# Performance work log

Hardware: AMD Instinct MI355X
Metric: run time of the kernel (lower is better)

The kernel has to match this reference:

```python
import jax, jax.numpy as jnp
import numpy as np

N = 100000      # nodes
E = 800000      # directed edges per branch
HID = 128
FOUT = 128
HEADS = 2
LAYERS = 3      # convlayer
JK_LAYERS = 3
H2 = (JK_LAYERS * HID) // 2   # PyG JK-LSTM hidden size = 192
N_AA = 26
N_SS = 3


def setup_inputs() -> dict:
    key = jax.random.key(0)
    ks = iter(jax.random.split(key, 32))
    def nrm(shape, scale=0.05):
        return jax.random.normal(next(ks), shape, dtype=jnp.float32) * scale
    return {
        "x_idx": jax.random.randint(next(ks), (N, 2), 0, N_SS),
        "x_flt": jax.random.normal(next(ks), (N, 5), dtype=jnp.float32),
        "edge_index_l": jax.random.randint(next(ks), (2, E), 0, N),
        "edge_index_r": jax.random.randint(next(ks), (2, E), 0, N),
        "emb_aa": nrm((2, N_AA, HID - 5)),          # [branch, vocab, hid-5]
        "emb_ss": nrm((2, N_SS, HID - 5)),
        "conv_W": nrm((2, LAYERS, HID, HEADS * HID)),
        "conv_att_src": nrm((2, LAYERS, HEADS, HID)),
        "conv_att_dst": nrm((2, LAYERS, HEADS, HID)),
        "conv_bias": nrm((2, LAYERS, HID)),
        "lstm_Wih": nrm((2, 2, 4 * H2, HID)),        # [branch, direction, 4H2, hid]
        "lstm_Whh": nrm((2, 2, 4 * H2, H2)),
        "lstm_bih": nrm((2, 2, 4 * H2)),
        "lstm_bhh": nrm((2, 2, 4 * H2)),
        "jk_att_W": nrm((2, 2 * H2)),
        "jk_att_b": nrm((2,)),
        "dummy_W": nrm((2, HID, HID)),
        "dummy_b": nrm((2, HID)),
        "fin_W": nrm((4, HID, FOUT)),
        "fin_b": nrm((4, FOUT)),
        "last_W": nrm((FOUT,)),                      # Linear(fout,1,bias=False)
    }


def _gat_conv(x, src, dst, W, att_src, att_dst, bias):
    # PyG GATConv, concat=False (mean over heads), leaky_relu slope 0.2
    n = x.shape[0]
    h, c = att_src.shape
    xh = (x @ W).reshape(n, h, c)                         # [N,H,C]
    a_src = jnp.einsum('nhc,hc->nh', xh, att_src)
    a_dst = jnp.einsum('nhc,hc->nh', xh, att_dst)
    e = jax.nn.leaky_relu(a_src[src] + a_dst[dst], 0.2)   # [E,H]
    m = jax.ops.segment_max(e, dst, num_segments=n)
    ex = jnp.exp(e - m[dst])
    denom = jax.ops.segment_sum(ex, dst, num_segments=n)
    alpha = ex / (denom[dst] + 1e-16)                     # segment softmax over dst
    out = jax.ops.segment_sum(xh[src] * alpha[:, :, None], dst, num_segments=n)
    return out.mean(axis=1) + bias                        # [N,C]


def _lstm_dir(xs, Wih, Whh, bih, bhh, reverse):
    # xs: [L,N,C]; single-layer LSTM, torch gate order i,f,g,o
    n = xs.shape[1]
    h2 = Whh.shape[1]
    b = bih + bhh
    def cell(carry, xt):
        h, c = carry
        g = xt @ Wih.T + h @ Whh.T + b
        i, f, gg, o = jnp.split(g, 4, axis=-1)
        c = jax.nn.sigmoid(f) * c + jax.nn.sigmoid(i) * jnp.tanh(gg)
        h = jax.nn.sigmoid(o) * jnp.tanh(c)
        return (h, c), h
    init = (jnp.zeros((n, h2), xs.dtype), jnp.zeros((n, h2), xs.dtype))
    _, hs = jax.lax.scan(cell, init, xs, reverse=reverse)
    return hs  # [L,N,H2]


def _jk(xs, Wih, Whh, bih, bhh, att_w, att_b):
    # PyG JumpingKnowledge('lstm'): bi-LSTM over layer axis + scalar attention
    hf = _lstm_dir(xs, Wih[0], Whh[0], bih[0], bhh[0], False)
    hb = _lstm_dir(xs, Wih[1], Whh[1], bih[1], bhh[1], True)
    h = jnp.concatenate([hf, hb], axis=-1)                # [L,N,2H2]
    a = jax.nn.softmax(jnp.einsum('lnh,h->ln', h, att_w) + att_b, axis=0)
    return (xs * a[..., None]).sum(axis=0)                # [N,C]


def _forward(x_idx, x_flt, edge_index_l, edge_index_r, emb_aa, emb_ss,
             conv_W, conv_att_src, conv_att_dst, conv_bias,
             lstm_Wih, lstm_Whh, lstm_bih, lstm_bhh, jk_att_W, jk_att_b,
             dummy_W, dummy_b, fin_W, fin_b, last_W):
    n = x_idx.shape[0]
    loops = jnp.arange(n)  # GATConv add_self_loops=True
    src_l = jnp.concatenate([edge_index_l[0], loops]); dst_l = jnp.concatenate([edge_index_l[1], loops])
    src_r = jnp.concatenate([edge_index_r[0], loops]); dst_r = jnp.concatenate([edge_index_r[1], loops])
    x_l = jnp.concatenate([emb_aa[0][x_idx[:, 0]] + emb_ss[0][x_idx[:, 1]], x_flt], axis=1)
    x_r = jnp.concatenate([emb_aa[1][x_idx[:, 0]] + emb_ss[1][x_idx[:, 1]], x_flt], axis=1)
    xs_l, xs_r = [], []
    for i in range(LAYERS):
        mean = (x_l + x_r) * 0.5
        o_l = mean + jax.nn.relu(_gat_conv(x_l, src_l, dst_l, conv_W[0, i], conv_att_src[0, i], conv_att_dst[0, i], conv_bias[0, i]))
        o_r = mean + jax.nn.relu(_gat_conv(x_r, src_r, dst_r, conv_W[1, i], conv_att_src[1, i], conv_att_dst[1, i], conv_bias[1, i]))
        x_l, x_r = o_l, o_r
        xs_l.append(x_l); xs_r.append(x_r)
    jk_l = _jk(jnp.stack(xs_l), lstm_Wih[0], lstm_Whh[0], lstm_bih[0], lstm_bhh[0], jk_att_W[0], jk_att_b[0])
    jk_r = _jk(jnp.stack(xs_r), lstm_Wih[1], lstm_Whh[1], lstm_bih[1], lstm_bhh[1], jk_att_W[1], jk_att_b[1])
    sq_l = jk_l @ dummy_W[0] + dummy_b[0]
    sq_r = jk_r @ dummy_W[1] + dummy_b[1]
    feats = [jk_l, sq_l, jk_r, sq_r]
    outs = [feats[i] @ fin_W[i] + fin_b[i] for i in range(4)]
    alpha = jax.nn.softmax(jnp.stack([o @ last_W for o in outs], axis=1), axis=1)  # [N,4]
    nodeemb = sum(outs[i] * alpha[:, i:i + 1] for i in range(4))
    return nodeemb


def reference(x_idx, x_flt, edge_index_l, edge_index_r, emb_aa, emb_ss,
              conv_W, conv_att_src, conv_att_dst, conv_bias,
              lstm_Wih, lstm_Whh, lstm_bih, lstm_bhh, jk_att_W, jk_att_b,
              dummy_W, dummy_b, fin_W, fin_b, last_W):
    return _forward(x_idx, x_flt, edge_index_l, edge_index_r, emb_aa, emb_ss,
                    conv_W, conv_att_src, conv_att_dst, conv_bias,
                    lstm_Wih, lstm_Whh, lstm_bih, lstm_bhh, jk_att_W, jk_att_b,
                    dummy_W, dummy_b, fin_W, fin_b, last_W)
```

## Files before the change

### kernel.cpp

```cpp
#include <hip/hip_runtime.h>
#include <cstddef>
#include <cstdint>

#define N_NODES 100000
#define N_EDGES 800000
#define EL_TOT  900000
#define HID 128
#define H2  192
#define G4  768
#define CH3 50000
#define BK  32
#define LDST 32
#define SCANB 98

typedef unsigned short bf16;
typedef __attribute__((ext_vector_type(8))) short bf16x8v;
typedef __attribute__((ext_vector_type(4))) float f32x4v;

#define AS1 __attribute__((address_space(1)))
#define AS3 __attribute__((address_space(3)))

__device__ __forceinline__ void async16(const bf16* g, bf16* l) {
    __builtin_amdgcn_global_load_lds((AS1 void*)g, (AS3 void*)l, 16, 0, 0);
}
// ... 109 lines not shown
        __syncthreads();
    }
    if (i < N_NODES) tmp[i] = sdata[threadIdx.x];
    if (threadIdx.x == 1023) bsums[b * SCANB + blockIdx.x] = sdata[1023];
}

__global__ void scan2_kernel(int* __restrict__ bsums) {
    int b = threadIdx.x;
    if (b < 2) {
        int c = 0;
        for (int k = 0; k < SCANB; ++k) {
            int t = bsums[b * SCANB + k];
            bsums[b * SCANB + k] = c;
            c += t;
        }
    }
}

__global__ void scan3_kernel(const int* __restrict__ bsums,
                             const int* __restrict__ deg0, const int* __restrict__ deg1,
                             const int* __restrict__ tmp0, const int* __restrict__ tmp1,
                             int* __restrict__ offs0, int* __restrict__ offs1,
                             int* __restrict__ pos0, int* __restrict__ pos1) {
    const int b = blockIdx.y;
    const int* deg = b ? deg1 : deg0;
    const int* tmp = b ? tmp1 : tmp0;
    int* offs = b ? offs1 : offs0;
    int* pos = b ? pos1 : pos0;
    int carry = bsums[b * SCANB + blockIdx.x];
    int i = blockIdx.x * 1024 + threadIdx.x;
    if (i < N_NODES) {
        int inc = tmp[i] + carry;
        offs[i + 1] = inc;
        pos[i] = inc - deg[i];
    }
    if (i == 0) offs[0] = 0;
}

__global__ void fill_kernel(const int* __restrict__ srcrow,
                            const int* __restrict__ dstrow,
                            int* __restrict__ pos, int* __restrict__ srcs) {
    int t = blockIdx.x * blockDim.x + threadIdx.x;
    if (t >= EL_TOT) return;
    int s, d;
    if (t < N_EDGES) { s = srcrow[t]; d = dstrow[t]; }
    else             { s = d = t - N_EDGES; }
    int p = atomicAdd(&pos[d], 1);
    srcs[p] = s;
}

template<typename TC>
__device__ __forceinline__ void gemm128_body(
    const bf16* __restrict__ A1, const bf16* __restrict__ B1, int K1,
    const bf16* __restrict__ A2, const bf16* __restrict__ B2, int K2,
    TC* __restrict__ C, const float* __restrict__ bias, int R, int M,
    int bm0, int bn0) {
    __shared__ bf16 As[2][128 * LDST];
    __shared__ bf16 Bs[2][128 * LDST];
    const int tid = threadIdx.x;
    const int lane = tid & 63;
    const int wave = tid >> 6;
    const int wm = (wave & 1) * 64, wn = (wave >> 1) * 64;
    const int l15 = lane & 15;
    const int q8 = (lane >> 4) * 8;
    const int lr = lane >> 2;
    const int lc = (lane & 3) * 8;

    f32x4v acc[4][4];
#pragma unroll
    for (int i = 0; i < 4; ++i)
#pragma unroll
        for (int j = 0; j < 4; ++j) acc[i][j] = (f32x4v)(0.0f);

    const int n1 = K1 / BK;
    const int n2 = A2 ? (K2 / BK) : 0;
    const int ns = n1 + n2;

    auto stage = [&](int buf, int s) {
        const bf16* Ap; const bf16* Bp; int K, k0;
        if (s < n1) { Ap = A1; Bp = B1; K = K1; k0 = s * BK; }
        else        { Ap = A2; Bp = B2; K = K2; k0 = (s - n1) * BK; }
#pragma unroll
        for (int rnd = 0; rnd < 2; ++rnd) {
            const int rbase = wave * 16 + rnd * 64;
            const int row = rbase + lr;
            int ga = bm0 + row; ga = (ga < R) ? ga : (R - 1);
            async16(Ap + (size_t)ga * K + k0 + lc, &As[buf][rbase * LDST]);
            async16(Bp + (size_t)(bn0 + row) * K + k0 + lc, &Bs[buf][rbase * LDST]);
        }
    };

    stage(0, 0);
    __syncthreads();
    for (int s = 0; s < ns; ++s) {
        const int cur = s & 1;
        if (s + 1 < ns) stage(cur ^ 1, s + 1);
        bf16x8v af[4], bfv[4];
#pragma unroll
        for (int i = 0; i < 4; ++i) {
            af[i]  = *(const bf16x8v*)&As[cur][(wm + i * 16 + l15) * LDST + q8];
            bfv[i] = *(const bf16x8v*)&Bs[cur][(wn + i * 16 + l15) * LDST + q8];
        }
#pragma unroll
        for (int i = 0; i < 4; ++i)
#pragma unroll
            for (int j = 0; j < 4; ++j)
                acc[i][j] = __builtin_amdgcn_mfma_f32_16x16x32_bf16(
                    af[i], bfv[j], acc[i][j], 0, 0, 0);
        __syncthreads();
    }

#pragma unroll
    for (int i = 0; i < 4; ++i) {
        const int row0 = bm0 + wm + i * 16 + (lane >> 4) * 4;
#pragma unroll
        for (int j = 0; j < 4; ++j) {
            const int col = bn0 + wn + j * 16 + l15;
            const float bv = bias ? bias[col] : 0.f;
#pragma unroll
            for (int r = 0; r < 4; ++r) {
                const int gr = row0 + r;
                if (gr < R) stE(C, (size_t)gr * M + col, acc[i][j][r] + bv);
            }
        }
    }
}

template<typename TC>
__global__ __launch_bounds__(256) void mfma_gemm_kernel(
    const bf16* __restrict__ A1, const bf16* __restrict__ B1, int K1,
    const bf16* __restrict__ A2, const bf16* __restrict__ B2, int K2,
    TC* __restrict__ C, const float* __restrict__ bias, int R, int M) {
    int bm0, nt;
    if (!swz_tile(R, M >> 7, bm0, nt)) return;
    gemm128_body<TC>(A1, B1, K1, A2, B2, K2, C, bias, R, M, bm0, nt * 128);
}

template<typename TC>
__global__ __launch_bounds__(256) void mfma_gemm_b_kernel(
    const bf16* a0, const bf16* a1, const bf16* a2, const bf16* a3,
    const bf16* __restrict__ Bbase,
    TC* c0, TC* c1, TC* c2, TC* c3,
    const float* __restrict__ bias, int R) {
    int bm0, nt;
    if (!swz_tile(R, 1, bm0, nt)) return;
    const int y = blockIdx.y;
    const bf16* A1 = (y == 0) ? a0 : (y == 1) ? a1 : (y == 2) ? a2 : a3;
    TC* C = (y == 0) ? c0 : (y == 1) ? c1 : (y == 2) ? c2 : c3;
    gemm128_body<TC>(A1, Bbase + (size_t)y * 128 * 128, 128,
                     nullptr, nullptr, 0, C,
                     bias + (size_t)y * 128, R, 128, bm0, 0);
}

__global__ __launch_bounds__(256) void lstm_gemm_kernel(
    const bf16* __restrict__ A1, const bf16* __restrict__ B1,
    const bf16* __restrict__ A2, const bf16* __restrict__ B2,
    const float* __restrict__ bias, bf16* __restrict__ c_state,
    bf16* __restrict__ h_out, const float* __restrict__ aw,
    float* __restrict__ score, int R) {
    __shared__ bf16 As[2][128 * LDST];
    __shared__ bf16 Bs[2][128 * LDST];
    int bm0, nt;
    if (!swz_tile(R, G4 >> 7, bm0, nt)) return;
    const int bn0 = nt * 128;
    const int tid = threadIdx.x;
    const int lane = tid & 63;
    const int wave = tid >> 6;
    const int wm = (wave & 1) * 64, wn = (wave >> 1) * 64;
    const int l15 = lane & 15;
    const int q = lane >> 4;
    const int q8 = q * 8;
    const int lr = lane >> 2;
    const int lc = (lane & 3) * 8;
    const bool first = (A2 == nullptr);

    f32x4v acc[4][4];
#pragma unroll
    for (int i = 0; i < 4; ++i)
#pragma unroll
        for (int j = 0; j < 4; ++j) acc[i][j] = (f32x4v)(0.0f);

    const int n1 = HID / BK;
    const int ns = n1 + (first ? 0 : (H2 / BK));

    auto stage = [&](int buf, int s) {
        const bf16* Ap; const bf16* Bp; int K, k0;
        if (s < n1) { Ap = A1; Bp = B1; K = HID; k0 = s * BK; }
        else        { Ap = A2; Bp = B2; K = H2;  k0 = (s - n1) * BK; }
#pragma unroll
        for (int rnd = 0; rnd < 2; ++rnd) {
            const int rbase = wave * 16 + rnd * 64;
            const int row = rbase + lr;
            int ga = bm0 + row; ga = (ga < R) ? ga : (R - 1);
            async16(Ap + (size_t)ga * K + k0 + lc, &As[buf][rbase * LDST]);
            async16(Bp + (size_t)(bn0 + row) * K + k0 + lc, &Bs[buf][rbase * LDST]);
        }
    };

    stage(0, 0);
    __syncthreads();
    for (int s = 0; s < ns; ++s) {
        const int cur = s & 1;
        if (s + 1 < ns) stage(cur ^ 1, s + 1);
        bf16x8v af[4], bfv[4];
#pragma unroll
        for (int i = 0; i < 4; ++i) {
            af[i]  = *(const bf16x8v*)&As[cur][(wm + i * 16 + l15) * LDST + q8];
            bfv[i] = *(const bf16x8v*)&Bs[cur][(wn + i * 16 + l15) * LDST + q8];
        }
#pragma unroll
        for (int i = 0; i < 4; ++i)
#pragma unroll
            for (int j = 0; j < 4; ++j)
                acc[i][j] = __builtin_amdgcn_mfma_f32_16x16x32_bf16(
                    af[i], bfv[j], acc[i][j], 0, 0, 0);
        __syncthreads();
    }

    const int u = ((bn0 + wn) >> 6) * 16 + l15;
    const float awu = aw[u];
    float bv[4];
#pragma unroll
    for (int j = 0; j < 4; ++j) bv[j] = bias[bn0 + wn + j * 16 + l15];
    float psum[4][4];
#pragma unroll
    for (int i = 0; i < 4; ++i) {
        const int row0 = bm0 + wm + i * 16 + q * 4;
#pragma unroll
        for (int r = 0; r < 4; ++r) {
            const int gr = row0 + r;
            const bool ok = gr < R;
            float ig = acc[i][0][r] + bv[0];
            float fg = acc[i][1][r] + bv[1];
            float gg = acc[i][2][r] + bv[2];
            float og = acc[i][3][r] + bv[3];
            float si = 1.f / (1.f + __expf(-ig));
            float sf = 1.f / (1.f + __expf(-fg));
            float so = 1.f / (1.f + __expf(-og));
            float co = (ok && !first) ? b2f(c_state[(size_t)gr * H2 + u]) : 0.f;
            float cn = sf * co + si * ftanh(gg);
            float hn = so * ftanh(cn);
            if (ok) {
                c_state[(size_t)gr * H2 + u] = f2b(cn);
                h_out[(size_t)gr * H2 + u] = f2b(hn);
            }
            psum[i][r] = hn * awu;
        }
    }
#pragma unroll
    for (int m = 1; m < 16; m <<= 1)
#pragma unroll
        for (int i = 0; i < 4; ++i)
#pragma unroll
            for (int r = 0; r < 4; ++r)
                psum[i][r] += __shfl_xor(psum[i][r], m);
    if (l15 == 0) {
#pragma unroll
        for (int i = 0; i < 4; ++i)
#pragma unroll
            for (int r = 0; r < 4; ++r) {
                const int gr = bm0 + wm + i * 16 + q * 4 + r;
                if (gr < R) atomicAdd(&score[gr], psum[i][r]);
            }
    }
}

__global__ __launch_bounds__(256) void mfma_gemm_x0_kernel(
    const int* __restrict__ xidx, const float* __restrict__ xflt,
    const float* __restrict__ embA, const float* __restrict__ embS,
    const bf16* __restrict__ B1, bf16* __restrict__ C, int R, int M) {
    __shared__ bf16 As[128 * LDST];
    __shared__ bf16 Bs[128 * LDST];
    int bm0, nt;
    if (!swz_tile(R, M >> 7, bm0, nt)) return;
    const int bn0 = nt * 128;
    const int tid = threadIdx.x;
    const int lane = tid & 63;
    const int wave = tid >> 6;
    const int wm = (wave & 1) * 64, wn = (wave >> 1) * 64;
    const int l15 = lane & 15;
    const int q8 = (lane >> 4) * 8;
    const int srow = tid >> 2;
    const int scol = (tid & 3) * 8;
    const int lr = lane >> 2;
    const int lc = (lane & 3) * 8;

    f32x4v acc[4][4];
#pragma unroll
    for (int i = 0; i < 4; ++i)
#pragma unroll
        for (int j = 0; j < 4; ++j) acc[i][j] = (f32x4v)(0.0f);

    for (int k0 = 0; k0 < 128; k0 += BK) {
#pragma unroll
        for (int rnd = 0; rnd < 2; ++rnd) {
            {
                int row = srow + rnd * 64;
                int ga = bm0 + row; ga = (ga < R) ? ga : (R - 1);
                int ia = xidx[2 * ga], is_ = xidx[2 * ga + 1];
                bf16 tmp[8];
#pragma unroll
                for (int t = 0; t < 8; ++t)
                    tmp[t] = f2b(x0_val(k0 + scol + t, ia, is_, ga, embA, embS, xflt));
                *(int4*)&As[row * LDST + scol] = *(const int4*)tmp;
            }
            {
                const int rbase = wave * 16 + rnd * 64;
                int row = rbase + lr;
                async16(B1 + (size_t)(bn0 + row) * 128 + k0 + lc, &Bs[rbase * LDST]);
            }
        }
        __syncthreads();
        bf16x8v af[4], bfv[4];
#pragma unroll
        for (int i = 0; i < 4; ++i) {
            af[i]  = *(const bf16x8v*)&As[(wm + i * 16 + l15) * LDST + q8];
            bfv[i] = *(const bf16x8v*)&Bs[(wn + i * 16 + l15) * LDST + q8];
        }
#pragma unroll
        for (int i = 0; i < 4; ++i)
#pragma unroll
            for (int j = 0; j < 4; ++j)
                acc[i][j] = __builtin_amdgcn_mfma_f32_16x16x32_bf16(
                    af[i], bfv[j], acc[i][j], 0, 0, 0);
        __syncthreads();
    }
#pragma unroll
    for (int i = 0; i < 4; ++i) {
        const int row0 = bm0 + wm + i * 16 + (lane >> 4) * 4;
#pragma unroll
        for (int j = 0; j < 4; ++j) {
            const int col = bn0 + wn + j * 16 + l15;
#pragma unroll
            for (int r = 0; r < 4; ++r) {
                const int gr = row0 + r;
                if (gr < R) C[(size_t)gr * M + col] = f2b(acc[i][j][r]);
            }
        }
    }
}


__global__ __launch_bounds__(256) void att_kernel(
    const bf16* __restrict__ xh, const float* __restrict__ as_,
    const float* __restrict__ ad_, float* __restrict__ asrc, float* __restrict__ adst) {
    int w = (blockIdx.x * blockDim.x + threadIdx.x) >> 6;
    int lane = threadIdx.x & 63;
    if (w >= N_NODES) return;
    const bf16* row = xh + (size_t)w * 256;
    float x0 = b2f(row[lane]), x1 = b2f(row[64 + lane]);
    float x2 = b2f(row[128 + lane]), x3 = b2f(row[192 + lane]);
    float s0 = x0 * as_[lane] + x1 * as_[64 + lane];
    float s1 = x2 * as_[128 + lane] + x3 * as_[192 + lane];
    float d0 = x0 * ad_[lane] + x1 * ad_[64 + lane];
    float d1 = x2 * ad_[128 + lane] + x3 * ad_[192 + lane];
    for (int o = 1; o < 64; o <<= 1) {
        s0 += __shfl_xor(s0, o); s1 += __shfl_xor(s1, o);
        d0 += __shfl_xor(d0, o); d1 += __shfl_xor(d1, o);
    }
    if (lane == 0) {
        asrc[2 * w] = s0; asrc[2 * w + 1] = s1;
        adst[2 * w] = d0; adst[2 * w + 1] = d1;
    }
}

__device__ __forceinline__ float lrelu02(float x) { return x > 0.f ? x : 0.2f * x; }

__global__ __launch_bounds__(256) void agg_kernel(
    const bf16* __restrict__ xh, const float* __restrict__ asrc,
    const float* __restrict__ adst, const int* __restrict__ offs,
    const int* __restrict__ srcs,
    const bf16* __restrict__ xprev_l, const bf16* __restrict__ xprev_r,
    const int* __restrict__ xidx, const float* __restrict__ xflt,
    const float* __restrict__ embAl, const float* __restrict__ embSl,
    const float* __restrict__ embAr, const float* __restrict__ embSr,
    const float* __restrict__ bias, bf16* __restrict__ outx) {
    int n = (blockIdx.x * blockDim.x + threadIdx.x) >> 6;
    int lane = threadIdx.x & 63;
    if (n >= N_NODES) return;
    const int start = offs[n], end = offs[n + 1];
    const float ad0 = adst[2 * n], ad1 = adst[2 * n + 1];

    const int eh = lane >> 5;
    const int l32 = lane & 31;
    const int head = l32 >> 4;
    const int l15 = l32 & 15;
    const int col = head * 128 + l15 * 8;
    const float adh = head ? ad1 : ad0;

    float acc[8] = {0.f, 0.f, 0.f, 0.f, 0.f, 0.f, 0.f, 0.f};
    float dsum = 0.f;
#pragma unroll 2
    for (int j = start; j < end; j += 2) {
        int e = j + eh;
        if (e < end) {
            int s = srcs[e];
            float a = asrc[2 * s + head] + adh;
            float al = __expf(lrelu02(a));
            if (l15 == 0) dsum += al;
            int4 v = *(const int4*)(xh + (size_t)s * 256 + col);
            const int* w = (const int*)&v;
#pragma unroll
            for (int t = 0; t < 4; ++t) {
                float lo = __uint_as_float(((unsigned)w[t]) << 16);
                float hi = __uint_as_float(((unsigned)w[t]) & 0xffff0000u);
                acc[2 * t]     += lo * al;
                acc[2 * t + 1] += hi * al;
            }
        }
    }
#pragma unroll
    for (int t = 0; t < 8; ++t) acc[t] += __shfl_xor(acc[t], 32);
    dsum += __shfl_xor(dsum, 32);
    float dh = __shfl(dsum, lane & 48);
    float invh = 1.f / (dh + 1e-16f);
#pragma unroll
    for (int t = 0; t < 8; ++t) {
        acc[t] *= invh;
        acc[t] = 0.5f * (acc[t] + __shfl_xor(acc[t], 16));
    }

    if (lane < 16) {
        const int c0 = lane * 8;
        const size_t base = (size_t)n * HID + c0;
        float xm[8];
        if (xidx) {
            int ia = xidx[2 * n], is_ = xidx[2 * n + 1];
#pragma unroll
            for (int t = 0; t < 8; ++t)
                xm[t] = 0.5f * (x0_val(c0 + t, ia, is_, n, embAl, embSl, xflt) +
                                x0_val(c0 + t, ia, is_, n, embAr, embSr, xflt));
        } else {
            int4 vl = *(const int4*)(xprev_l + base);
            int4 vr = *(const int4*)(xprev_r + base);
            const int* wl = (const int*)&vl;
            const int* wr = (const int*)&vr;
#pragma unroll
            for (int t = 0; t < 4; ++t) {
                xm[2 * t] = 0.5f * (__uint_as_float(((unsigned)wl[t]) << 16) +
                                    __uint_as_float(((unsigned)wr[t]) << 16));
                xm[2 * t + 1] = 0.5f * (__uint_as_float(((unsigned)wl[t]) & 0xffff0000u) +
                                        __uint_as_float(((unsigned)wr[t]) & 0xffff0000u));
            }
        }
        bf16 res[8];
#pragma unroll
        for (int t = 0; t < 8; ++t)
            res[t] = f2b(xm[t] + fmaxf(0.f, acc[t] + bias[c0 + t]));
        *(int4*)(outx + base) = *(const int4*)res;
    }
}


__global__ __launch_bounds__(256) void jkfin_kernel(
    const float* __restrict__ sb, const bf16* __restrict__ xs0,
    const bf16* __restrict__ xs1, const bf16* __restrict__ xs2,
    bf16* __restrict__ jk) {
    int w = (blockIdx.x * blockDim.x + threadIdx.x) >> 6;
    int lane = threadIdx.x & 63;
    if (w >= N_NODES) return;
    float s0 = sb[w], s1 = sb[N_NODES + w], s2 = sb[2 * N_NODES + w];
    float m = fmaxf(s0, fmaxf(s1, s2));
    float a0 = __expf(s0 - m), a1 = __expf(s1 - m), a2 = __expf(s2 - m);
    float inv = 1.f / (a0 + a1 + a2);
    a0 *= inv; a1 *= inv; a2 *= inv;
    size_t gn = (size_t)w * HID + lane * 2;
#pragma unroll
    for (int t = 0; t < 2; ++t) {
        float v0 = b2f(xs0[gn + t]);
        float v1 = b2f(xs1[gn + t]);
        float v2 = b2f(xs2[gn + t]);
        jk[gn + t] = f2b(v0 * a0 + v1 * a1 + v2 * a2);
    }
}

__global__ __launch_bounds__(256) void final_kernel(
    const float* __restrict__ o0, const float* __restrict__ o1,
    const float* __restrict__ o2, const float* __restrict__ o3,
    const float* __restrict__ lw, float* __restrict__ out, int nloc, long long c3off) {
    int w = (blockIdx.x * blockDim.x + threadIdx.x) >> 6;
    int lane = threadIdx.x & 63;
    if (w >= nloc) return;
    size_t base = (size_t)w * HID;
    float w0 = lw[lane], w1 = lw[64 + lane];
    const float* op[4] = {o0, o1, o2, o3};
    float v[4][2];
    float s[4];
#pragma unroll
    for (int i = 0; i < 4; ++i) {
        v[i][0] = op[i][base + lane];
        v[i][1] = op[i][base + 64 + lane];
        float t = v[i][0] * w0 + v[i][1] * w1;
        for (int o = 1; o < 64; o <<= 1) t += __shfl_xor(t, o);
        s[i] = t;
    }
    float m = fmaxf(fmaxf(s[0], s[1]), fmaxf(s[2], s[3]));
    float e0 = __expf(s[0] - m), e1 = __expf(s[1] - m);
    float e2 = __expf(s[2] - m), e3 = __expf(s[3] - m);
    float inv = 1.f / (e0 + e1 + e2 + e3);
    float r0 = (v[0][0] * e0 + v[1][0] * e1 + v[2][0] * e2 + v[3][0] * e3) * inv;
    float r1 = (v[0][1] * e0 + v[1][1] * e1 + v[2][1] * e2 + v[3][1] * e3) * inv;
    size_t obase = (size_t)(c3off + w) * HID;
    out[obase + lane] = r0;
    out[obase + 64 + lane] = r1;
}


static long long align1k(long long x) { return (x + 1023) & ~1023LL; }

extern "C" void kernel_launch(void* const* d_in, const int* in_sizes, int n_in,
                              void* d_out, int out_size, void* d_ws, size_t ws_size,
                              hipStream_t stream) {
    (void)in_sizes; (void)n_in; (void)out_size;
    const int*   x_idx   = (const int*)  d_in[0];
    const float* x_flt   = (const float*)d_in[1];
    const int*   ei_l    = (const int*)  d_in[2];
    const int*   ei_r    = (const int*)  d_in[3];
    const float* emb_aa  = (const float*)d_in[4];
    const float* emb_ss  = (const float*)d_in[5];
    const float* conv_W  = (const float*)d_in[6];
    const float* att_s   = (const float*)d_in[7];
    const float* att_d   = (const float*)d_in[8];
    const float* conv_b  = (const float*)d_in[9];
    const float* Wih     = (const float*)d_in[10];
    const float* Whh     = (const float*)d_in[11];
    const float* bih     = (const float*)d_in[12];
    const float* bhh     = (const float*)d_in[13];
    const float* jkw     = (const float*)d_in[14];
    const float* dummy_W = (const float*)d_in[16];
    const float* dummy_b = (const float*)d_in[17];
    const float* fin_W   = (const float*)d_in[18];
    const float* fin_b   = (const float*)d_in[19];
    const float* last_W  = (const float*)d_in[20];
    float* out = (float*)d_out;

    const long long S = (long long)N_NODES * HID;
    char* ws = (char*)d_ws;
    long long off = 0;

    bf16* hist = (bf16*)(ws + off);  off += align1k(6 * S * 2);
    float* scores = (float*)(ws + off); off += align1k(6LL * N_NODES * 4);
    float* bsum   = (float*)(ws + off); off += align1k(4LL * G4 * 4);
    int* bsums    = (int*)(ws + off);  off += align1k(2LL * SCANB * 4);
    bf16* Wih_b   = (bf16*)(ws + off); off += align1k(4LL * G4 * HID * 2);
    bf16* Whh_b   = (bf16*)(ws + off); off += align1k(4LL * G4 * H2 * 2);
    bf16* dummyWt = (bf16*)(ws + off); off += align1k(2LL * 128 * 128 * 2);
    bf16* finWt   = (bf16*)(ws + off); off += align1k(4LL * 128 * 128 * 2);

    char* BIG = ws + off;
    const long long slot0 = align1k(2 * S * 2);
    const long long slot1 = align1k((long long)N_NODES * H2 * 2);
    const long long need = off + slot0 + slot1;

    if ((long long)ws_size < need) {
        float val = 200000.0f + (float)(ws_size >> 20);
        sentinel_kernel<<<(N_NODES * HID + 255) / 256, 256, 0, stream>>>(
            out, N_NODES * HID, val);
        return;
    }

    bf16* xh  = (bf16*)BIG;
    bf16* jkb = (bf16*)BIG;
    int* ibase = (int*)(BIG + slot0);
    int *deg[2], *offs[2], *pos[2], *srcs[2];
    long long io = 0;
    for (int b = 0; b < 2; ++b) {
        deg[b]  = ibase + io; io += N_NODES;
        offs[b] = ibase + io; io += N_NODES + 1;
        pos[b]  = ibase + io; io += N_NODES;
        srcs[b] = ibase + io; io += EL_TOT;
    }
    long long io4a = ((io * 4 + 15) & ~15LL);
    float* asrc = (float*)(BIG + slot0 + io4a);
    float* adst = asrc + 2LL * N_NODES;
    bf16* convWt = (bf16*)(BIG + slot0 + io4a + 4LL * N_NODES * 4);
    bf16* hA = (bf16*)BIG;
    bf16* hB = (bf16*)d_out;
    bf16* cC = (bf16*)(BIG + slot0);

    const float* embA[2] = {emb_aa, emb_aa + 26 * 123};
    const float* embS[2] = {emb_ss, emb_ss + 3 * 123};

    bsum_perm_kernel<<<12, 256, 0, stream>>>(bih, bhh, bsum);
    trans_kernel<<<(6 * 128 * 256 + 255) / 256, 256, 0, stream>>>(
        conv_W, convWt, 6, 128, 256);
    lstm_w_perm_kernel<<<(4 * G4 * HID + 255) / 256, 256, 0, stream>>>(
        Wih, Wih_b, HID);
    lstm_w_perm_kernel<<<(4 * G4 * H2 + 255) / 256, 256, 0, stream>>>(
        Whh, Whh_b, H2);
    trans_kernel<<<(2 * 128 * 128 + 255) / 256, 256, 0, stream>>>(
        dummy_W, dummyWt, 2, 128, 128);
    trans_kernel<<<(4 * 128 * 128 + 255) / 256, 256, 0, stream>>>(
        fin_W, finWt, 4, 128, 128);
    hipMemsetAsync(deg[0], 0, N_NODES * sizeof(int), stream);
    hipMemsetAsync(deg[1], 0, N_NODES * sizeof(int), stream);
    deg_kernel<<<(EL_TOT + 255) / 256, 256, 0, stream>>>(ei_l + N_EDGES, deg[0]);
    deg_kernel<<<(EL_TOT + 255) / 256, 256, 0, stream>>>(ei_r + N_EDGES, deg[1]);
    scan1_kernel<<<dim3(SCANB, 2), 1024, 0, stream>>>(
        deg[0], deg[1], pos[0], pos[1], bsums);
    scan2_kernel<<<1, 64, 0, stream>>>(bsums);
    scan3_kernel<<<dim3(SCANB, 2), 1024, 0, stream>>>(
        bsums, deg[0], deg[1], pos[0], pos[1], offs[0], offs[1], pos[0], pos[1]);
    fill_kernel<<<(EL_TOT + 255) / 256, 256, 0, stream>>>(
        ei_l, ei_l + N_EDGES, pos[0], srcs[0]);
    fill_kernel<<<(EL_TOT + 255) / 256, 256, 0, stream>>>(
        ei_r, ei_r + N_EDGES, pos[1], srcs[1]);

    for (int i = 0; i < 3; ++i) {
        for (int b = 0; b < 2; ++b) {
            const bf16* Wc = convWt + (size_t)(b * 3 + i) * 256 * 128;
            if (i == 0) {
                mfma_gemm_x0_kernel<<<swz_grid(N_NODES, 2), 256, 0, stream>>>(
                    x_idx, x_flt, embA[b], embS[b], Wc, xh, N_NODES, 256);
            } else {
                mfma_gemm_kernel<bf16><<<swz_grid(N_NODES, 2), 256, 0, stream>>>(
                    hist + (size_t)(b * 3 + i - 1) * S, Wc, 128,
                    nullptr, nullptr, 0, xh, nullptr, N_NODES, 256);
            }
            att_kernel<<<25000, 256, 0, stream>>>(
                xh, att_s + (size_t)(b * 3 + i) * 2 * HID,
                att_d + (size_t)(b * 3 + i) * 2 * HID, asrc, adst);
            const bf16* xpl = (i == 0) ? nullptr : hist + (size_t)(i - 1) * S;
            const bf16* xpr = (i == 0) ? nullptr : hist + (size_t)(3 + i - 1) * S;
            agg_kernel<<<25000, 256, 0, stream>>>(
                xh, asrc, adst, offs[b], srcs[b], xpl, xpr,
                (i == 0) ? x_idx : nullptr, x_flt,
                embA[0], embS[0], embA[1], embS[1],
                conv_b + (size_t)(b * 3 + i) * HID, hist + (size_t)(b * 3 + i) * S);
        }
    }

    hipMemsetAsync(scores, 0, (size_t)6 * N_NODES * 4, stream);
    const int gx = swz_grid(N_NODES, 6);
    for (int b = 0; b < 2; ++b) {
        for (int dir = 0; dir < 2; ++dir) {
            const bf16* Wi = Wih_b + (size_t)(b * 2 + dir) * G4 * HID;
            const bf16* Wh = Whh_b + (size_t)(b * 2 + dir) * G4 * H2;
            const float* bs = bsum + (size_t)(b * 2 + dir) * G4;
            const float* aw = jkw + (size_t)b * 2 * H2 + (size_t)dir * H2;
            for (int st = 0; st < 3; ++st) {
                int l = dir ? (2 - st) : st;
                const bf16* A = hist + (size_t)(b * 3 + l) * S;
                const bf16* hin = (st == 0) ? nullptr : ((st & 1) ? hA : hB);
                bf16* hout = (st & 1) ? hB : hA;
                lstm_gemm_kernel<<<gx, 256, 0, stream>>>(
                    A, Wi, hin, Wh, bs, cC, hout, aw,
                    scores + (size_t)(b * 3 + l) * N_NODES, N_NODES);
            }
        }
    }
    for (int b = 0; b < 2; ++b)
        jkfin_kernel<<<25000, 256, 0, stream>>>(
            scores + (size_t)b * 3 * N_NODES,
            hist + (size_t)b * 3 * S, hist + (size_t)(b * 3 + 1) * S,
            hist + (size_t)(b * 3 + 2) * S, jkb + (size_t)b * S);

    float* f3 = (float*)hist;
    bf16* jkl = jkb; bf16* jkr = jkb + S;
    for (long long c3 = 0; c3 < N_NODES; c3 += CH3) {
        int Rr = (int)((N_NODES - c3) < CH3 ? (N_NODES - c3) : CH3);
        float* o0 = f3;
        float* o1 = f3 + 1LL * CH3 * HID;
        float* o2 = f3 + 2LL * CH3 * HID;
        float* o3 = f3 + 3LL * CH3 * HID;
        bf16* sql = (bf16*)(f3 + 4LL * CH3 * HID);
        bf16* sqr = sql + (long long)CH3 * HID;
        mfma_gemm_b_kernel<bf16><<<dim3(swz_grid(Rr, 1), 2), 256, 0, stream>>>(
            jkl + c3 * HID, jkr + c3 * HID, nullptr, nullptr,
            dummyWt, sql, sqr, nullptr, nullptr, dummy_b, Rr);
        mfma_gemm_b_kernel<float><<<dim3(swz_grid(Rr, 1), 4), 256, 0, stream>>>(
            jkl + c3 * HID, sql, jkr + c3 * HID, sqr,
            finWt, o0, o1, o2, o3, fin_b, Rr);
        final_kernel<<<(Rr + 3) / 4, 256, 0, stream>>>(
            o0, o1, o2, o3, last_W, out, Rr, c3);
    }
}
```

Baseline: 3.014 ms.

## Fuse attention logits into aggregation and batch LSTM directions per launch

Removes the separate att_kernel. The aggregation kernel now recomputes the per-edge source attention logit from the gathered source row and the destination logit from the node's own row, and each wave processes four edges at a time across both heads. The LSTM GEMM launches are also merged so the forward and backward directions of a branch run in one 2-D grid, when the workspace is large enough to hold separate state buffers per direction. The cost is redundant dot products and shuffles on every edge, plus higher register pressure in the aggregation kernel.

```diff
diff --git a/kernel.cpp b/kernel.cpp
--- a/kernel.cpp
+++ b/kernel.cpp
@@ -285,17 +285,32 @@
                      bias + (size_t)y * 128, R, 128, bm0, 0);
 }
 
-__global__ __launch_bounds__(256) void lstm_gemm_kernel(
-    const bf16* __restrict__ A1, const bf16* __restrict__ B1,
-    const bf16* __restrict__ A2, const bf16* __restrict__ B2,
-    const float* __restrict__ bias, bf16* __restrict__ c_state,
-    bf16* __restrict__ h_out, const float* __restrict__ aw,
-    float* __restrict__ score, int R) {
+__global__ __launch_bounds__(256) void lstm_gemm2_kernel(
+    const bf16* __restrict__ Ax0, const bf16* __restrict__ Ax1,
+    const bf16* __restrict__ Wi, const bf16* __restrict__ Wh,
+    const float* __restrict__ biasB,
+    bf16* __restrict__ cS0, bf16* __restrict__ cS1,
+    const bf16* __restrict__ hin0, const bf16* __restrict__ hin1,
+    bf16* __restrict__ hout0, bf16* __restrict__ hout1,
+    const float* __restrict__ awB,
+    float* __restrict__ score0, float* __restrict__ score1,
+    int first, int R) {
     __shared__ bf16 As[2][128 * LDST];
     __shared__ bf16 Bs[2][128 * LDST];
     int bm0, nt;
     if (!swz_tile(R, G4 >> 7, bm0, nt)) return;
     const int bn0 = nt * 128;
+    const int y = blockIdx.y;
+    const bf16* A1 = y ? Ax1 : Ax0;
+    const bf16* B1 = Wi + (size_t)y * G4 * HID;
+    const bf16* A2 = y ? hin1 : hin0;
+    const bf16* B2 = Wh + (size_t)y * G4 * H2;
+    const float* bias = biasB + (size_t)y * G4;
+    bf16* c_state = y ? cS1 : cS0;
+    bf16* h_out = y ? hout1 : hout0;
+    const float* aw = awB + (size_t)y * H2;
+    float* score = y ? score1 : score0;
+
     const int tid = threadIdx.x;
     const int lane = tid & 63;
     const int wave = tid >> 6;
@@ -305,7 +320,6 @@
     const int q8 = q * 8;
     const int lr = lane >> 2;
     const int lc = (lane & 3) * 8;
-    const bool first = (A2 == nullptr);
 
     f32x4v acc[4][4];
 #pragma unroll
@@ -474,34 +488,11 @@
 }
 
 
-__global__ __launch_bounds__(256) void att_kernel(
+__device__ __forceinline__ float lrelu02(float x) { return x > 0.f ? x : 0.2f * x; }
+
+__global__ __launch_bounds__(256) void agg_kernel(
     const bf16* __restrict__ xh, const float* __restrict__ as_,
-    const float* __restrict__ ad_, float* __restrict__ asrc, float* __restrict__ adst) {
-    int w = (blockIdx.x * blockDim.x + threadIdx.x) >> 6;
-    int lane = threadIdx.x & 63;
-    if (w >= N_NODES) return;
-    const bf16* row = xh + (size_t)w * 256;
-    float x0 = b2f(row[lane]), x1 = b2f(row[64 + lane]);
-    float x2 = b2f(row[128 + lane]), x3 = b2f(row[192 + lane]);
-    float s0 = x0 * as_[lane] + x1 * as_[64 + lane];
-    float s1 = x2 * as_[128 + lane] + x3 * as_[192 + lane];
-    float d0 = x0 * ad_[lane] + x1 * ad_[64 + lane];
-    float d1 = x2 * ad_[128 + lane] + x3 * ad_[192 + lane];
-    for (int o = 1; o < 64; o <<= 1) {
-        s0 += __shfl_xor(s0, o); s1 += __shfl_xor(s1, o);
-        d0 += __shfl_xor(d0, o); d1 += __shfl_xor(d1, o);
-    }
-    if (lane == 0) {
-        asrc[2 * w] = s0; asrc[2 * w + 1] = s1;
-        adst[2 * w] = d0; adst[2 * w + 1] = d1;
-    }
-}
-
-__device__ __forceinline__ float lrelu02(float x) { return x > 0.f ? x : 0.2f * x; }
-
-__global__ __launch_bounds__(256) void agg_kernel(
-    const bf16* __restrict__ xh, const float* __restrict__ asrc,
-    const float* __restrict__ adst, const int* __restrict__ offs,
+    const float* __restrict__ ad_, const int* __restrict__ offs,
     const int* __restrict__ srcs,
     const bf16* __restrict__ xprev_l, const bf16* __restrict__ xprev_r,
     const int* __restrict__ xidx, const float* __restrict__ xflt,
@@ -512,49 +503,84 @@
     int lane = threadIdx.x & 63;
     if (n >= N_NODES) return;
     const int start = offs[n], end = offs[n + 1];
-    const float ad0 = adst[2 * n], ad1 = adst[2 * n + 1];
-
-    const int eh = lane >> 5;
-    const int l32 = lane & 31;
-    const int head = l32 >> 4;
-    const int l15 = l32 & 15;
-    const int col = head * 128 + l15 * 8;
-    const float adh = head ? ad1 : ad0;
-
-    float acc[8] = {0.f, 0.f, 0.f, 0.f, 0.f, 0.f, 0.f, 0.f};
-    float dsum = 0.f;
+    const int l15 = lane & 15;
+    const int g = lane >> 4;
+
+    float av0[8], av1[8];
+#pragma unroll
+    for (int t = 0; t < 8; ++t) {
+        av0[t] = as_[l15 * 8 + t];
+        av1[t] = as_[128 + l15 * 8 + t];
+    }
+
+    float d0, d1;
+    {
+        uint2 v = *(const uint2*)(xh + (size_t)n * 256 + lane * 4);
+        float p = ad_[lane * 4 + 0] * b2f((bf16)(v.x & 0xffffu))
+                + ad_[lane * 4 + 1] * b2f((bf16)(v.x >> 16))
+                + ad_[lane * 4 + 2] * b2f((bf16)(v.y & 0xffffu))
+                + ad_[lane * 4 + 3] * b2f((bf16)(v.y >> 16));
+        for (int o = 1; o < 32; o <<= 1) p += __shfl_xor(p, o);
+        d0 = __shfl(p, 0);
+        d1 = __shfl(p, 32);
+    }
+
+    float acc0[8] = {0, 0, 0, 0, 0, 0, 0, 0};
+    float acc1[8] = {0, 0, 0, 0, 0, 0, 0, 0};
+    float ds0 = 0.f, ds1 = 0.f;
 #pragma unroll 2
-    for (int j = start; j < end; j += 2) {
-        int e = j + eh;
+    for (int j = start; j < end; j += 4) {
+        int e = j + g;
         if (e < end) {
             int s = srcs[e];
-            float a = asrc[2 * s + head] + adh;
-            float al = __expf(lrelu02(a));
-            if (l15 == 0) dsum += al;
-            int4 v = *(const int4*)(xh + (size_t)s * 256 + col);
-            const int* w = (const int*)&v;
+            const bf16* row = xh + (size_t)s * 256 + l15 * 8;
+            int4 v0 = *(const int4*)row;
+            int4 v1 = *(const int4*)(row + 128);
+            const int* w0 = (const int*)&v0;
+            const int* w1 = (const int*)&v1;
+            float x0[8], x1[8];
 #pragma unroll
             for (int t = 0; t < 4; ++t) {
-                float lo = __uint_as_float(((unsigned)w[t]) << 16);
-                float hi = __uint_as_float(((unsigned)w[t]) & 0xffff0000u);
-                acc[2 * t]     += lo * al;
-                acc[2 * t + 1] += hi * al;
-            }
-        }
-    }
-#pragma unroll
-    for (int t = 0; t < 8; ++t) acc[t] += __shfl_xor(acc[t], 32);
-    dsum += __shfl_xor(dsum, 32);
-    float dh = __shfl(dsum, lane & 48);
-    float invh = 1.f / (dh + 1e-16f);
+                x0[2 * t]     = __uint_as_float(((unsigned)w0[t]) << 16);
+                x0[2 * t + 1] = __uint_as_float(((unsigned)w0[t]) & 0xffff0000u);
+                x1[2 * t]     = __uint_as_float(((unsigned)w1[t]) << 16);
+                x1[2 * t + 1] = __uint_as_float(((unsigned)w1[t]) & 0xffff0000u);
+            }
+            float p0 = 0.f, p1 = 0.f;
+#pragma unroll
+            for (int t = 0; t < 8; ++t) { p0 += av0[t] * x0[t]; p1 += av1[t] * x1[t]; }
+#pragma unroll
+            for (int m = 1; m < 16; m <<= 1) {
+                p0 += __shfl_xor(p0, m);
+                p1 += __shfl_xor(p1, m);
+            }
+            float al0 = __expf(lrelu02(p0 + d0));
+            float al1 = __expf(lrelu02(p1 + d1));
+            if (l15 == 0) { ds0 += al0; ds1 += al1; }
+#pragma unroll
+            for (int t = 0; t < 8; ++t) {
+                acc0[t] += x0[t] * al0;
+                acc1[t] += x1[t] * al1;
+            }
+        }
+    }
 #pragma unroll
     for (int t = 0; t < 8; ++t) {
-        acc[t] *= invh;
-        acc[t] = 0.5f * (acc[t] + __shfl_xor(acc[t], 16));
-    }
+        acc0[t] += __shfl_xor(acc0[t], 16); acc0[t] += __shfl_xor(acc0[t], 32);
+        acc1[t] += __shfl_xor(acc1[t], 16); acc1[t] += __shfl_xor(acc1[t], 32);
+    }
+    ds0 += __shfl_xor(ds0, 16); ds0 += __shfl_xor(ds0, 32);
+    ds1 += __shfl_xor(ds1, 16); ds1 += __shfl_xor(ds1, 32);
+    ds0 = __shfl(ds0, 0); ds1 = __shfl(ds1, 0);
+    const float inv0 = 1.f / (ds0 + 1e-16f);
+    const float inv1 = 1.f / (ds1 + 1e-16f);
+    float accm[8];
+#pragma unroll
+    for (int t = 0; t < 8; ++t)
+        accm[t] = 0.5f * (acc0[t] * inv0 + acc1[t] * inv1);
 
     if (lane < 16) {
-        const int c0 = lane * 8;
+        const int c0 = l15 * 8;
         const size_t base = (size_t)n * HID + c0;
         float xm[8];
         if (xidx) {
@@ -579,7 +605,7 @@
         bf16 res[8];
 #pragma unroll
         for (int t = 0; t < 8; ++t)
-            res[t] = f2b(xm[t] + fmaxf(0.f, acc[t] + bias[c0 + t]));
+            res[t] = f2b(xm[t] + fmaxf(0.f, accm[t] + bias[c0 + t]));
         *(int4*)(outx + base) = *(const int4*)res;
     }
 }
@@ -683,14 +709,17 @@
     char* BIG = ws + off;
     const long long slot0 = align1k(2 * S * 2);
     const long long slot1 = align1k((long long)N_NODES * H2 * 2);
-    const long long need = off + slot0 + slot1;
-
-    if ((long long)ws_size < need) {
+    const long long HS    = slot1;
+    const long long need_seq = off + slot0 + slot1;
+    const long long need_tB  = off + 5 * HS;
+
+    if ((long long)ws_size < need_seq) {
         float val = 200000.0f + (float)(ws_size >> 20);
         sentinel_kernel<<<(N_NODES * HID + 255) / 256, 256, 0, stream>>>(
             out, N_NODES * HID, val);
         return;
     }
+    const bool tierB = (long long)ws_size >= need_tB;
 
     bf16* xh  = (bf16*)BIG;
     bf16* jkb = (bf16*)BIG;
@@ -704,12 +733,16 @@
         srcs[b] = ibase + io; io += EL_TOT;
     }
     long long io4a = ((io * 4 + 15) & ~15LL);
-    float* asrc = (float*)(BIG + slot0 + io4a);
-    float* adst = asrc + 2LL * N_NODES;
-    bf16* convWt = (bf16*)(BIG + slot0 + io4a + 4LL * N_NODES * 4);
+    bf16* convWt = (bf16*)(BIG + slot0 + io4a);
     bf16* hA = (bf16*)BIG;
     bf16* hB = (bf16*)d_out;
     bf16* cC = (bf16*)(BIG + slot0);
+    bf16* cB0 = (bf16*)BIG;
+    bf16* cB1 = (bf16*)(BIG + HS);
+    bf16* hX0 = (bf16*)(BIG + 2 * HS);
+    bf16* hX1 = (bf16*)(BIG + 3 * HS);
+    bf16* hY0 = (bf16*)(BIG + 4 * HS);
+    bf16* hY1 = (bf16*)d_out;
 
     const float* embA[2] = {emb_aa, emb_aa + 26 * 123};
     const float* embS[2] = {emb_ss, emb_ss + 3 * 123};
@@ -750,13 +783,12 @@
                     hist + (size_t)(b * 3 + i - 1) * S, Wc, 128,
                     nullptr, nullptr, 0, xh, nullptr, N_NODES, 256);
             }
-            att_kernel<<<25000, 256, 0, stream>>>(
-                xh, att_s + (size_t)(b * 3 + i) * 2 * HID,
-                att_d + (size_t)(b * 3 + i) * 2 * HID, asrc, adst);
             const bf16* xpl = (i == 0) ? nullptr : hist + (size_t)(i - 1) * S;
             const bf16* xpr = (i == 0) ? nullptr : hist + (size_t)(3 + i - 1) * S;
             agg_kernel<<<25000, 256, 0, stream>>>(
-                xh, asrc, adst, offs[b], srcs[b], xpl, xpr,
+                xh, att_s + (size_t)(b * 3 + i) * 2 * HID,
+                att_d + (size_t)(b * 3 + i) * 2 * HID,
+                offs[b], srcs[b], xpl, xpr,
                 (i == 0) ? x_idx : nullptr, x_flt,
                 embA[0], embS[0], embA[1], embS[1],
                 conv_b + (size_t)(b * 3 + i) * HID, hist + (size_t)(b * 3 + i) * S);
@@ -765,20 +797,44 @@
 
     hipMemsetAsync(scores, 0, (size_t)6 * N_NODES * 4, stream);
     const int gx = swz_grid(N_NODES, 6);
-    for (int b = 0; b < 2; ++b) {
-        for (int dir = 0; dir < 2; ++dir) {
-            const bf16* Wi = Wih_b + (size_t)(b * 2 + dir) * G4 * HID;
-            const bf16* Wh = Whh_b + (size_t)(b * 2 + dir) * G4 * H2;
-            const float* bs = bsum + (size_t)(b * 2 + dir) * G4;
-            const float* aw = jkw + (size_t)b * 2 * H2 + (size_t)dir * H2;
+    if (tierB) {
+        for (int b = 0; b < 2; ++b) {
+            const int c0 = b * 2;
             for (int st = 0; st < 3; ++st) {
-                int l = dir ? (2 - st) : st;
-                const bf16* A = hist + (size_t)(b * 3 + l) * S;
-                const bf16* hin = (st == 0) ? nullptr : ((st & 1) ? hA : hB);
-                bf16* hout = (st & 1) ? hB : hA;
-                lstm_gemm_kernel<<<gx, 256, 0, stream>>>(
-                    A, Wi, hin, Wh, bs, cC, hout, aw,
-                    scores + (size_t)(b * 3 + l) * N_NODES, N_NODES);
+                const int l0 = st, l1 = 2 - st;
+                const bf16 *hin0, *hin1; bf16 *ho0, *ho1;
+                if (st == 0)      { hin0 = hin1 = nullptr; ho0 = hX0; ho1 = hX1; }
+                else if (st == 1) { hin0 = hX0; hin1 = hX1; ho0 = hY0; ho1 = hY1; }
+                else              { hin0 = hY0; hin1 = hY1; ho0 = hX0; ho1 = hX1; }
+                lstm_gemm2_kernel<<<dim3(gx, 2), 256, 0, stream>>>(
+                    hist + (size_t)(b * 3 + l0) * S, hist + (size_t)(b * 3 + l1) * S,
+                    Wih_b + (size_t)c0 * G4 * HID, Whh_b + (size_t)c0 * G4 * H2,
+                    bsum + (size_t)c0 * G4,
+                    cB0, cB1, hin0, hin1, ho0, ho1,
+                    jkw + (size_t)b * 2 * H2,
+                    scores + (size_t)(b * 3 + l0) * N_NODES,
+                    scores + (size_t)(b * 3 + l1) * N_NODES,
+                    st == 0 ? 1 : 0, N_NODES);
+            }
+        }
+    } else {
+        for (int b = 0; b < 2; ++b) {
+            for (int dir = 0; dir < 2; ++dir) {
+                const int combo = b * 2 + dir;
+                for (int st = 0; st < 3; ++st) {
+                    int l = dir ? (2 - st) : st;
+                    const bf16* hin = (st == 0) ? nullptr : ((st & 1) ? hA : hB);
+                    bf16* hout = (st & 1) ? hB : hA;
+                    lstm_gemm2_kernel<<<dim3(gx, 1), 256, 0, stream>>>(
+                        hist + (size_t)(b * 3 + l) * S, nullptr,
+                        Wih_b + (size_t)combo * G4 * HID,
+                        Whh_b + (size_t)combo * G4 * H2,
+                        bsum + (size_t)combo * G4,
+                        cC, nullptr, hin, nullptr, hout, nullptr,
+                        jkw + (size_t)b * 2 * H2 + (size_t)dir * H2,
+                        scores + (size_t)(b * 3 + l) * N_NODES, nullptr,
+                        st == 0 ? 1 : 0, N_NODES);
+                }
             }
         }
     }
```

After: 2.998 ms. No clear change (-0.5%).

## Fuse dst-attention into aggregation, process both heads per edge, skip last LSTM stores

Applied to the files above, without the earlier changes.

Removes the destination-attention dot product and its buffer from att_kernel and recomputes it inside agg_kernel from the node's own xh row. The aggregation loop is restructured so each lane group handles one edge for both heads (4 edges in flight per wave instead of 2 edges split by head), loading asrc as a float2. The LSTM kernel gets explicit first/last flags and skips writing c_state and h_out on the final step, which nothing reads. The unused second-operand path in gemm128_body is also removed.

```diff
diff --git a/kernel.cpp b/kernel.cpp
--- a/kernel.cpp
+++ b/kernel.cpp
@@ -185,7 +185,6 @@
 template<typename TC>
 __device__ __forceinline__ void gemm128_body(
     const bf16* __restrict__ A1, const bf16* __restrict__ B1, int K1,
-    const bf16* __restrict__ A2, const bf16* __restrict__ B2, int K2,
     TC* __restrict__ C, const float* __restrict__ bias, int R, int M,
     int bm0, int bn0) {
     __shared__ bf16 As[2][128 * LDST];
@@ -205,21 +204,16 @@
 #pragma unroll
         for (int j = 0; j < 4; ++j) acc[i][j] = (f32x4v)(0.0f);
 
-    const int n1 = K1 / BK;
-    const int n2 = A2 ? (K2 / BK) : 0;
-    const int ns = n1 + n2;
-
+    const int ns = K1 / BK;
     auto stage = [&](int buf, int s) {
-        const bf16* Ap; const bf16* Bp; int K, k0;
-        if (s < n1) { Ap = A1; Bp = B1; K = K1; k0 = s * BK; }
-        else        { Ap = A2; Bp = B2; K = K2; k0 = (s - n1) * BK; }
+        const int k0 = s * BK;
 #pragma unroll
         for (int rnd = 0; rnd < 2; ++rnd) {
             const int rbase = wave * 16 + rnd * 64;
             const int row = rbase + lr;
             int ga = bm0 + row; ga = (ga < R) ? ga : (R - 1);
-            async16(Ap + (size_t)ga * K + k0 + lc, &As[buf][rbase * LDST]);
-            async16(Bp + (size_t)(bn0 + row) * K + k0 + lc, &Bs[buf][rbase * LDST]);
+            async16(A1 + (size_t)ga * K1 + k0 + lc, &As[buf][rbase * LDST]);
+            async16(B1 + (size_t)(bn0 + row) * K1 + k0 + lc, &Bs[buf][rbase * LDST]);
         }
     };
 
@@ -262,11 +256,10 @@
 template<typename TC>
 __global__ __launch_bounds__(256) void mfma_gemm_kernel(
     const bf16* __restrict__ A1, const bf16* __restrict__ B1, int K1,
-    const bf16* __restrict__ A2, const bf16* __restrict__ B2, int K2,
     TC* __restrict__ C, const float* __restrict__ bias, int R, int M) {
     int bm0, nt;
     if (!swz_tile(R, M >> 7, bm0, nt)) return;
-    gemm128_body<TC>(A1, B1, K1, A2, B2, K2, C, bias, R, M, bm0, nt * 128);
+    gemm128_body<TC>(A1, B1, K1, C, bias, R, M, bm0, nt * 128);
 }
 
 template<typename TC>
@@ -280,8 +273,7 @@
     const int y = blockIdx.y;
     const bf16* A1 = (y == 0) ? a0 : (y == 1) ? a1 : (y == 2) ? a2 : a3;
     TC* C = (y == 0) ? c0 : (y == 1) ? c1 : (y == 2) ? c2 : c3;
-    gemm128_body<TC>(A1, Bbase + (size_t)y * 128 * 128, 128,
-                     nullptr, nullptr, 0, C,
+    gemm128_body<TC>(A1, Bbase + (size_t)y * 128 * 128, 128, C,
                      bias + (size_t)y * 128, R, 128, bm0, 0);
 }
 
@@ -290,7 +282,7 @@
     const bf16* __restrict__ A2, const bf16* __restrict__ B2,
     const float* __restrict__ bias, bf16* __restrict__ c_state,
     bf16* __restrict__ h_out, const float* __restrict__ aw,
-    float* __restrict__ score, int R) {
+    float* __restrict__ score, int first, int last, int R) {
     __shared__ bf16 As[2][128 * LDST];
     __shared__ bf16 Bs[2][128 * LDST];
     int bm0, nt;
@@ -305,7 +297,6 @@
     const int q8 = q * 8;
     const int lr = lane >> 2;
     const int lc = (lane & 3) * 8;
-    const bool first = (A2 == nullptr);
 
     f32x4v acc[4][4];
 #pragma unroll
@@ -373,7 +364,7 @@
             float co = (ok && !first) ? b2f(c_state[(size_t)gr * H2 + u]) : 0.f;
             float cn = sf * co + si * ftanh(gg);
             float hn = so * ftanh(cn);
-            if (ok) {
+            if (ok && !last) {
                 c_state[(size_t)gr * H2 + u] = f2b(cn);
                 h_out[(size_t)gr * H2 + u] = f2b(hn);
             }
@@ -476,7 +467,7 @@
 
 __global__ __launch_bounds__(256) void att_kernel(
     const bf16* __restrict__ xh, const float* __restrict__ as_,
-    const float* __restrict__ ad_, float* __restrict__ asrc, float* __restrict__ adst) {
+    float* __restrict__ asrc) {
     int w = (blockIdx.x * blockDim.x + threadIdx.x) >> 6;
     int lane = threadIdx.x & 63;
     if (w >= N_NODES) return;
@@ -485,15 +476,11 @@
     float x2 = b2f(row[128 + lane]), x3 = b2f(row[192 + lane]);
     float s0 = x0 * as_[lane] + x1 * as_[64 + lane];
     float s1 = x2 * as_[128 + lane] + x3 * as_[192 + lane];
-    float d0 = x0 * ad_[lane] + x1 * ad_[64 + lane];
-    float d1 = x2 * ad_[128 + lane] + x3 * ad_[192 + lane];
     for (int o = 1; o < 64; o <<= 1) {
         s0 += __shfl_xor(s0, o); s1 += __shfl_xor(s1, o);
-        d0 += __shfl_xor(d0, o); d1 += __shfl_xor(d1, o);
     }
     if (lane == 0) {
         asrc[2 * w] = s0; asrc[2 * w + 1] = s1;
-        adst[2 * w] = d0; adst[2 * w + 1] = d1;
     }
 }
 
@@ -501,7 +488,7 @@
 
 __global__ __launch_bounds__(256) void agg_kernel(
     const bf16* __restrict__ xh, const float* __restrict__ asrc,
-    const float* __restrict__ adst, const int* __restrict__ offs,
+    const float* __restrict__ ad_, const int* __restrict__ offs,
     const int* __restrict__ srcs,
     const bf16* __restrict__ xprev_l, const bf16* __restrict__ xprev_r,
     const int* __restrict__ xidx, const float* __restrict__ xflt,
@@ -512,49 +499,64 @@
     int lane = threadIdx.x & 63;
     if (n >= N_NODES) return;
     const int start = offs[n], end = offs[n + 1];
-    const float ad0 = adst[2 * n], ad1 = adst[2 * n + 1];
-
-    const int eh = lane >> 5;
-    const int l32 = lane & 31;
-    const int head = l32 >> 4;
-    const int l15 = l32 & 15;
-    const int col = head * 128 + l15 * 8;
-    const float adh = head ? ad1 : ad0;
-
-    float acc[8] = {0.f, 0.f, 0.f, 0.f, 0.f, 0.f, 0.f, 0.f};
-    float dsum = 0.f;
+    const int l15 = lane & 15;
+    const int g = lane >> 4;
+
+    float d0, d1;
+    {
+        uint2 v = *(const uint2*)(xh + (size_t)n * 256 + lane * 4);
+        float p = ad_[lane * 4 + 0] * b2f((bf16)(v.x & 0xffffu))
+                + ad_[lane * 4 + 1] * b2f((bf16)(v.x >> 16))
+                + ad_[lane * 4 + 2] * b2f((bf16)(v.y & 0xffffu))
+                + ad_[lane * 4 + 3] * b2f((bf16)(v.y >> 16));
+        for (int o = 1; o < 32; o <<= 1) p += __shfl_xor(p, o);
+        d0 = __shfl(p, 0);
+        d1 = __shfl(p, 32);
+    }
+
+    float acc0[8] = {0, 0, 0, 0, 0, 0, 0, 0};
+    float acc1[8] = {0, 0, 0, 0, 0, 0, 0, 0};
+    float ds0 = 0.f, ds1 = 0.f;
 #pragma unroll 2
-    for (int j = start; j < end; j += 2) {
-        int e = j + eh;
+    for (int j = start; j < end; j += 4) {
+        int e = j + g;
         if (e < end) {
             int s = srcs[e];
-            float a = asrc[2 * s + head] + adh;
-            float al = __expf(lrelu02(a));
-            if (l15 == 0) dsum += al;
-            int4 v = *(const int4*)(xh + (size_t)s * 256 + col);
-            const int* w = (const int*)&v;
+            float2 a2 = *(const float2*)(asrc + 2 * s);
+            float al0 = __expf(lrelu02(a2.x + d0));
+            float al1 = __expf(lrelu02(a2.y + d1));
+            if (l15 == 0) { ds0 += al0; ds1 += al1; }
+            const bf16* row = xh + (size_t)s * 256 + l15 * 8;
+            int4 v0 = *(const int4*)row;
+            int4 v1 = *(const int4*)(row + 128);
+            const int* w0 = (const int*)&v0;
+            const int* w1 = (const int*)&v1;
 #pragma unroll
             for (int t = 0; t < 4; ++t) {
-                float lo = __uint_as_float(((unsigned)w[t]) << 16);
-                float hi = __uint_as_float(((unsigned)w[t]) & 0xffff0000u);
-                acc[2 * t]     += lo * al;
-                acc[2 * t + 1] += hi * al;
-            }
-        }
-    }
-#pragma unroll
-    for (int t = 0; t < 8; ++t) acc[t] += __shfl_xor(acc[t], 32);
-    dsum += __shfl_xor(dsum, 32);
-    float dh = __shfl(dsum, lane & 48);
-    float invh = 1.f / (dh + 1e-16f);
+                acc0[2 * t]     += __uint_as_float(((unsigned)w0[t]) << 16) * al0;
+                acc0[2 * t + 1] += __uint_as_float(((unsigned)w0[t]) & 0xffff0000u) * al0;
+                acc1[2 * t]     += __uint_as_float(((unsigned)w1[t]) << 16) * al1;
+                acc1[2 * t + 1] += __uint_as_float(((unsigned)w1[t]) & 0xffff0000u) * al1;
+            }
+        }
+    }
 #pragma unroll
     for (int t = 0; t < 8; ++t) {
-        acc[t] *= invh;
-        acc[t] = 0.5f * (acc[t] + __shfl_xor(acc[t], 16));
-    }
+        acc0[t] += __shfl_xor(acc0[t], 16); acc0[t] += __shfl_xor(acc0[t], 32);
+        acc1[t] += __shfl_xor(acc1[t], 16); acc1[t] += __shfl_xor(acc1[t], 32);
+    }
+    ds0 += __shfl_xor(ds0, 16); ds0 += __shfl_xor(ds0, 32);
+    ds1 += __shfl_xor(ds1, 16); ds1 += __shfl_xor(ds1, 32);
+    ds0 = __shfl(ds0, 0); ds1 = __shfl(ds1, 0);
+    const float inv0 = 1.f / (ds0 + 1e-16f);
+    const float inv1 = 1.f / (ds1 + 1e-16f);
+    float accm[8];
+#pragma unroll
+    for (int t = 0; t < 8; ++t)
+        accm[t] = 0.5f * (acc0[t] * inv0 + acc1[t] * inv1);
 
     if (lane < 16) {
-        const int c0 = lane * 8;
+        const int c0 = l15 * 8;
         const size_t base = (size_t)n * HID + c0;
         float xm[8];
         if (xidx) {
@@ -579,7 +581,7 @@
         bf16 res[8];
 #pragma unroll
         for (int t = 0; t < 8; ++t)
-            res[t] = f2b(xm[t] + fmaxf(0.f, acc[t] + bias[c0 + t]));
+            res[t] = f2b(xm[t] + fmaxf(0.f, accm[t] + bias[c0 + t]));
         *(int4*)(outx + base) = *(const int4*)res;
     }
 }
@@ -705,8 +707,7 @@
     }
     long long io4a = ((io * 4 + 15) & ~15LL);
     float* asrc = (float*)(BIG + slot0 + io4a);
-    float* adst = asrc + 2LL * N_NODES;
-    bf16* convWt = (bf16*)(BIG + slot0 + io4a + 4LL * N_NODES * 4);
+    bf16* convWt = (bf16*)(BIG + slot0 + io4a + 2LL * N_NODES * 4);
     bf16* hA = (bf16*)BIG;
     bf16* hB = (bf16*)d_out;
     bf16* cC = (bf16*)(BIG + slot0);
@@ -748,15 +749,15 @@
             } else {
                 mfma_gemm_kernel<bf16><<<swz_grid(N_NODES, 2), 256, 0, stream>>>(
                     hist + (size_t)(b * 3 + i - 1) * S, Wc, 128,
-                    nullptr, nullptr, 0, xh, nullptr, N_NODES, 256);
+                    xh, nullptr, N_NODES, 256);
             }
             att_kernel<<<25000, 256, 0, stream>>>(
-                xh, att_s + (size_t)(b * 3 + i) * 2 * HID,
-                att_d + (size_t)(b * 3 + i) * 2 * HID, asrc, adst);
+                xh, att_s + (size_t)(b * 3 + i) * 2 * HID, asrc);
             const bf16* xpl = (i == 0) ? nullptr : hist + (size_t)(i - 1) * S;
             const bf16* xpr = (i == 0) ? nullptr : hist + (size_t)(3 + i - 1) * S;
             agg_kernel<<<25000, 256, 0, stream>>>(
-                xh, asrc, adst, offs[b], srcs[b], xpl, xpr,
+                xh, asrc, att_d + (size_t)(b * 3 + i) * 2 * HID,
+                offs[b], srcs[b], xpl, xpr,
                 (i == 0) ? x_idx : nullptr, x_flt,
                 embA[0], embS[0], embA[1], embS[1],
                 conv_b + (size_t)(b * 3 + i) * HID, hist + (size_t)(b * 3 + i) * S);
@@ -767,9 +768,10 @@
     const int gx = swz_grid(N_NODES, 6);
     for (int b = 0; b < 2; ++b) {
         for (int dir = 0; dir < 2; ++dir) {
-            const bf16* Wi = Wih_b + (size_t)(b * 2 + dir) * G4 * HID;
-            const bf16* Wh = Whh_b + (size_t)(b * 2 + dir) * G4 * H2;
-            const float* bs = bsum + (size_t)(b * 2 + dir) * G4;
+            const int combo = b * 2 + dir;
+            const bf16* Wi = Wih_b + (size_t)combo * G4 * HID;
+            const bf16* Wh = Whh_b + (size_t)combo * G4 * H2;
+            const float* bs = bsum + (size_t)combo * G4;
             const float* aw = jkw + (size_t)b * 2 * H2 + (size_t)dir * H2;
             for (int st = 0; st < 3; ++st) {
                 int l = dir ? (2 - st) : st;
@@ -778,7 +780,8 @@
                 bf16* hout = (st & 1) ? hB : hA;
                 lstm_gemm_kernel<<<gx, 256, 0, stream>>>(
                     A, Wi, hin, Wh, bs, cC, hout, aw,
-                    scores + (size_t)(b * 3 + l) * N_NODES, N_NODES);
+                    scores + (size_t)(b * 3 + l) * N_NODES,
+                    st == 0 ? 1 : 0, st == 2 ? 1 : 0, N_NODES);
             }
         }
     }
```

Measured after the change: 2.897 ms. 3.9% less time.
